# Kernel optimization log

Hardware: AMD Instinct MI355X
Metric: run time of the kernel (lower is better)

The kernel has to match this reference:

```python
import jax, jax.numpy as jnp
import numpy as np

D_MODEL = 1024
D_STATE = 16
EXPAND = 2
D_INNER = D_MODEL * EXPAND
BATCH = 512
SEQ = 100
DT = 0.01


def setup_inputs() -> dict:
    key = jax.random.key(0)
    ks = jax.random.split(key, 12)
    s = 0.02
    log_ts = jnp.linspace(jnp.log(0.001), jnp.log(0.1), D_STATE).reshape(1, D_STATE)
    return {
        "x": jax.random.normal(ks[0], (BATCH, SEQ, D_MODEL), jnp.float32),
        "pos_emb": jax.random.normal(ks[1], (1, 100, D_MODEL), jnp.float32),
        "W_in": jax.random.normal(ks[2], (D_INNER, D_MODEL), jnp.float32) * s,
        "b_in": jnp.zeros((D_INNER,), jnp.float32),
        "W_gate": jax.random.normal(ks[3], (D_INNER, D_MODEL), jnp.float32) * s,
        "b_gate": jnp.zeros((D_INNER,), jnp.float32),
        "A_log": log_ts.astype(jnp.float32),
        "W_B": jax.random.normal(ks[4], (D_STATE, D_INNER), jnp.float32) * s,
        "b_B": jnp.zeros((D_STATE,), jnp.float32),
        "W_C": jax.random.normal(ks[5], (D_STATE, D_MODEL), jnp.float32) * s,
        "b_C": jnp.zeros((D_STATE,), jnp.float32),
        "W_out": jax.random.normal(ks[6], (D_MODEL, D_INNER), jnp.float32) * s,
        "b_out": jnp.zeros((D_MODEL,), jnp.float32),
    }


def reference(x, pos_emb, W_in, b_in, W_gate, b_gate, A_log, W_B, b_B, W_C, b_C, W_out, b_out):
    b, s, _ = x.shape
    d_inner = W_in.shape[0]
    d_state = A_log.shape[-1]
    x = x + pos_emb[:, :s, :]
    x_proj = jnp.einsum("bsd,id->bsi", x, W_in) + b_in
    gate = jax.nn.sigmoid(jnp.einsum("bsd,id->bsi", x, W_gate) + b_gate)
    x_gated = x_proj * gate
    B = jnp.einsum("bsi,ni->bsn", x_gated, W_B) + b_B   # (b, s, d_state)
    C = jnp.einsum("bsd,nd->bsn", x, W_C) + b_C         # (b, s, d_state)
    A = jnp.exp(DT * jnp.exp(A_log))                      # (1, d_state), broadcasts over batch

    def step(h, bc):
        Bt, Ct = bc
        h = A * h + Bt
        return h, h * Ct

    h0 = jnp.zeros((b, d_state), x.dtype)
    _, ys = jax.lax.scan(step, h0, (jnp.swapaxes(B, 0, 1), jnp.swapaxes(C, 0, 1)))
    y = jnp.swapaxes(ys, 0, 1)                            # (b, s, d_state)
    d_slice = min(d_state, d_inner)
    expanded = jnp.pad(y[:, :, :d_slice], ((0, 0), (0, 0), (0, d_inner - d_slice)))
    return jnp.einsum("bsi,di->bsd", expanded, W_out) + b_out
```

## Files before the change

### kernel.cpp

```cpp
#include <hip/hip_runtime.h>
#include <hip/hip_bf16.h>
#include <stdint.h>

typedef unsigned short u16;
typedef u16   u16x8 __attribute__((ext_vector_type(8)));
typedef short s16x8 __attribute__((ext_vector_type(8)));
typedef float f32x4 __attribute__((ext_vector_type(4)));

#define TOKENS 51200
#define DMODEL 1024
#define DINNER 2048
#define NSTATE 16
#define SEQLEN 100

#define OFF_XP    0ull
#define OFF_WCAT  104857600ull
#define OFF_WB    113246208ull
#define OFF_WC    113311744ull
#define OFF_BPART 113344512ull
#define OFF_BFIN  165773312ull
#define OFF_CBUF  169050112ull
#define OFF_Y     172326912ull

__device__ __forceinline__ u16 f2b(float f) {
  uint32_t u = __float_as_uint(f);
  uint32_t r = (u + 0x7fffu + ((u >> 16) & 1u)) >> 16;
  return (u16)r;
}
__device__ __forceinline__ float b2f(u16 u) {
  return __uint_as_float(((uint32_t)u) << 16);
}

#define GLL(gp, lp) __builtin_amdgcn_global_load_lds( \
    (__attribute__((address_space(1))) unsigned int*)(gp), \
    (__attribute__((address_space(3))) unsigned int*)(lp), 16, 0, 0)
#define SB0() __builtin_amdgcn_sched_barrier(0)

__global__ void k_prep_x(const float* __restrict__ x, const float* __restrict__ pos,
                         u16* __restrict__ xp) {
  long e = ((long)blockIdx.x * blockDim.x + threadIdx.x) * 8;
  int d = (int)(e & (DMODEL - 1));
  long tok = e >> 10;
  int s = (int)(tok % SEQLEN);
  f32x4 a0 = *(const f32x4*)(x + e);
  f32x4 a1 = *(const f32x4*)(x + e + 4);
  f32x4 p0 = *(const f32x4*)(pos + (size_t)s * DMODEL + d);
  f32x4 p1 = *(const f32x4*)(pos + (size_t)s * DMODEL + d + 4);
  u16x8 o;
  o[0] = f2b(a0[0] + p0[0]); o[1] = f2b(a0[1] + p0[1]);
  o[2] = f2b(a0[2] + p0[2]); o[3] = f2b(a0[3] + p0[3]);
  o[4] = f2b(a1[0] + p1[0]); o[5] = f2b(a1[1] + p1[1]);
  o[6] = f2b(a1[2] + p1[2]); o[7] = f2b(a1[3] + p1[3]);
  *(u16x8*)(xp + e) = o;
}

__global__ void k_prep_w(const float* __restrict__ Win, const float* __restrict__ Wg,
                         u16* __restrict__ w2) {
  long e = ((long)blockIdx.x * blockDim.x + threadIdx.x) * 8;
  int r = (int)(e >> 10), c = (int)(e & 1023);
  int srow = ((r >> 5) << 4) + (r & 15);
  const float* src = ((r & 16) ? Wg : Win) + (size_t)srow * DMODEL + c;
  f32x4 a0 = *(const f32x4*)src;
  f32x4 a1 = *(const f32x4*)(src + 4);
  u16x8 o;
  o[0] = f2b(a0[0]); o[1] = f2b(a0[1]); o[2] = f2b(a0[2]); o[3] = f2b(a0[3]);
  o[4] = f2b(a1[0]); o[5] = f2b(a1[1]); o[6] = f2b(a1[2]); o[7] = f2b(a1[3]);
  *(u16x8*)(w2 + e) = o;
}

__global__ void k_prep_wbc(const float* __restrict__ WB, const float* __restrict__ WC,
                           u16* __restrict__ wb, u16* __restrict__ wc) {
  long e = ((long)blockIdx.x * blockDim.x + threadIdx.x) * 8;
  const float* src; u16* dst;
  if (e < 32768) { src = WB + e; dst = wb + e; }
  else           { src = WC + (e - 32768); dst = wc + (e - 32768); }
  f32x4 a0 = *(const f32x4*)src;
  f32x4 a1 = *(const f32x4*)(src + 4);
  u16x8 o;
  o[0] = f2b(a0[0]); o[1] = f2b(a0[1]); o[2] = f2b(a0[2]); o[3] = f2b(a0[3]);
  o[4] = f2b(a1[0]); o[5] = f2b(a1[1]); o[6] = f2b(a1[2]); o[7] = f2b(a1[3]);
  *(u16x8*)(dst) = o;
}

__global__ __launch_bounds__(512, 4) void k_gemm256(
    const u16* __restrict__ XP, const u16* __restrict__ W2, const u16* __restrict__ WBb,
    const float* __restrict__ b_in, const float* __restrict__ b_gate,
    float* __restrict__ Bpart) {
  extern __shared__ __align__(16) u16 smem[];
  char* smemc = (char*)smem;

  const int tid = threadIdx.x;
  const int bid = blockIdx.x;
  const int xcd = bid & 7;
  const int q   = bid >> 3;
  const int rb  = xcd * 50 + (q >> 4);
  const int nb  = q & 15;
  const int m0 = rb << 7;
  const int n0 = nb << 8;

  const int srow = tid >> 2;
  const int csrc = ((tid & 3) ^ ((tid >> 3) & 3)) << 3;
  const u16* gA = XP + (size_t)(m0 + srow) * DMODEL + csrc;
  const u16* gB = W2 + (size_t)(n0 + srow) * DMODEL + csrc;
  const int ldst = tid << 3;

  const int wid = tid >> 6, lane = tid & 63;
  const int wm = wid >> 2, wn = wid & 3;
  const int l15 = lane & 15, lhi = lane >> 4;
  const int arow0 = (wm << 6) + l15;
  const int brow0 = (wn << 6) + l15;
  const int kchA = (lhi ^ ((arow0 >> 1) & 3)) << 4;
  const int kchB = (lhi ^ ((brow0 >> 1) & 3)) << 4;

  auto rdA = [&](int bufb, int m) -> s16x8 {
    return *(const s16x8*)(smemc + bufb + ((arow0 + (m << 4)) << 6) + kchA);
  };
  auto rdB = [&](int bufb, int n) -> s16x8 {
    return *(const s16x8*)(smemc + bufb + 8192 + ((brow0 + (n << 4)) << 6) + kchB);
  };
  auto stage = [&](int t) {
    const int bb = (t & 1) << 14;
    const u16* a_ = gA + ((size_t)t << 5);
    const u16* b_ = gB + ((size_t)t << 5);
    GLL(a_,          smem + bb + ldst);
    GLL(b_,          smem + bb + 4096 + ldst);
    GLL(b_ + 131072, smem + bb + 8192 + ldst);
  };

  f32x4 acc[4][4] = {};

  stage(0); stage(1);

#pragma unroll 1
  for (int t = 0; t < 32; ++t) {
    if (t == 31) asm volatile("s_waitcnt vmcnt(0)" ::: "memory");
    else         asm volatile("s_waitcnt vmcnt(3)" ::: "memory");
    SB0();
    asm volatile("s_barrier" ::: "memory");
    SB0();
    const int bufb = (t & 1) << 15;

    s16x8 a[4], b[4];
#pragma unroll
    for (int m = 0; m < 4; ++m) a[m] = rdA(bufb, m);
#pragma unroll
    for (int n = 0; n < 4; ++n) b[n] = rdB(bufb, n);

    __builtin_amdgcn_s_setprio(1);
#pragma unroll
    for (int m = 0; m < 4; ++m)
#pragma unroll
      for (int n = 0; n < 2; ++n)
        acc[m][n] = __builtin_amdgcn_mfma_f32_16x16x32_bf16(a[m], b[n], acc[m][n], 0, 0, 0);
    __builtin_amdgcn_s_setprio(0);

    asm volatile("s_waitcnt lgkmcnt(0)" ::: "memory");
    SB0();
    asm volatile("s_barrier" ::: "memory");
    SB0();
    if (t < 30) stage(t + 2);
    SB0();

    __builtin_amdgcn_s_setprio(1);
#pragma unroll
    for (int m = 0; m < 4; ++m)
#pragma unroll
      for (int n = 2; n < 4; ++n)
        acc[m][n] = __builtin_amdgcn_mfma_f32_16x16x32_bf16(a[m], b[n], acc[m][n], 0, 0, 0);
    __builtin_amdgcn_s_setprio(0);
  }

  asm volatile("s_waitcnt lgkmcnt(0)" ::: "memory");
  SB0();
  asm volatile("s_barrier" ::: "memory");
  SB0();

  u16* xg = smem;
  float bi[2], bg[2];
#pragma unroll
  for (int u = 0; u < 2; ++u) {
    const int gcol = (nb << 7) + (((wn << 1) + u) << 4) + l15;
    bi[u] = b_in[gcol];
    bg[u] = b_gate[gcol];
  }
#pragma unroll
  for (int m = 0; m < 4; ++m)
#pragma unroll
    for (int u = 0; u < 2; ++u)
#pragma unroll
      for (int j = 0; j < 4; ++j) {
        const int row = (wm << 6) + (m << 4) + (lhi << 2) + j;
        const int col = (((wn << 1) + u) << 4) + l15;
        float pv = acc[m][2 * u][j] + bi[u];
        float gv = acc[m][2 * u + 1][j] + bg[u];
        xg[row * 136 + col] = f2b(pv / (1.0f + __expf(-gv)));
      }
  asm volatile("s_waitcnt lgkmcnt(0)" ::: "memory");
  asm volatile("s_barrier" ::: "memory");

  f32x4 bacc = {};
#pragma unroll
  for (int kc = 0; kc < 4; ++kc) {
    s16x8 av = *(const s16x8*)(xg + ((wid << 4) + l15) * 136 + (kc << 5) + (lhi << 3));
    s16x8 bv = *(const s16x8*)(WBb + (size_t)l15 * DINNER + (nb << 7) + (kc << 5) + (lhi << 3));
    bacc = __builtin_amdgcn_mfma_f32_16x16x32_bf16(av, bv, bacc, 0, 0, 0);
  }
  float* outp = Bpart + ((size_t)nb * TOKENS + m0 + (wid << 4) + (lhi << 2)) * NSTATE + l15;
#pragma unroll
  for (int j = 0; j < 4; ++j) outp[j * NSTATE] = bacc[j];
}

__global__ __launch_bounds__(256) void k_C(const u16* __restrict__ XP, const u16* __restrict__ WC,
                                           const float* __restrict__ bC, float* __restrict__ Cb) {
  __shared__ __align__(16) u16 wcl[16 * 1032];
  const int tid = threadIdx.x;
  const int m0 = blockIdx.x << 6;
#pragma unroll
  for (int i = 0; i < 8; ++i) {
    int c = i * 256 + tid;
    int row = c >> 7, col = c & 127;
    *(u16x8*)(wcl + row * 1032 + (col << 3)) = *(const u16x8*)(WC + (row << 10) + (col << 3));
  }
  __syncthreads();
  const int wv = tid >> 6, lane = tid & 63;
  const int l15 = lane & 15, lhi = lane >> 4;
  const u16* xr = XP + (size_t)(m0 + (wv << 4) + l15) * DMODEL + (lhi << 3);
  const u16* wr = wcl + l15 * 1032 + (lhi << 3);
  f32x4 acc = {};
#pragma unroll
  for (int t = 0; t < 32; ++t) {
    s16x8 av = *(const s16x8*)(xr + t * 32);
    s16x8 bv = *(const s16x8*)(wr + t * 32);
    acc = __builtin_amdgcn_mfma_f32_16x16x32_bf16(av, bv, acc, 0, 0, 0);
  }
  const float bc = bC[l15];
  float* o = Cb + (size_t)(m0 + (wv << 4) + (lhi << 2)) * NSTATE + l15;
#pragma unroll
  for (int j = 0; j < 4; ++j) o[j * NSTATE] = acc[j] + bc;
}

__global__ void k_finB(const float* __restrict__ Bpart, const float* __restrict__ bB,
                       float* __restrict__ Bf) {
  const long i = (long)blockIdx.x * blockDim.x + threadIdx.x;
  f32x4 s = {};
#pragma unroll
  for (int cb = 0; cb < 16; ++cb)
    s += *(const f32x4*)(Bpart + (size_t)cb * (TOKENS * NSTATE) + i * 4);
  s += *(const f32x4*)(bB + ((i & 3) << 2));
  *(f32x4*)(Bf + i * 4) = s;
}

__global__ void k_scan(const float* __restrict__ Bf, const float* __restrict__ Cb,
                       const float* __restrict__ Alog, float* __restrict__ Y) {
  const int t = threadIdx.x;
  const int b = blockIdx.x * 16 + (t >> 4);
  const int n = t & 15;
  const float A = __expf(0.01f * __expf(Alog[n]));
  float h = 0.f;
  const size_t base = (size_t)b * SEQLEN * NSTATE + n;
  for (int s = 0; s < SEQLEN; ++s) {
    const size_t idx = base + (size_t)s * NSTATE;
    h = A * h + Bf[idx];
    Y[idx] = h * Cb[idx];
  }
}

__global__ __launch_bounds__(256) void k_out(const float* __restrict__ Y,
                                             const float* __restrict__ Wout,
                                             const float* __restrict__ bout,
                                             float* __restrict__ out) {
  __shared__ float ys[32][16];
  const int tid = threadIdx.x;
  const long t0 = (long)blockIdx.x * 32;
  for (int i = tid; i < 512; i += 256) ys[i >> 4][i & 15] = Y[t0 * 16 + i];
  const int d0 = tid << 2;
  float w[4][16];
#pragma unroll
  for (int j = 0; j < 4; ++j)
#pragma unroll
    for (int q = 0; q < 4; ++q) {
      f32x4 wv = *(const f32x4*)(Wout + (size_t)(d0 + j) * DINNER + q * 4);
#pragma unroll
      for (int e = 0; e < 4; ++e) w[j][q * 4 + e] = wv[e];
    }
  f32x4 bo = *(const f32x4*)(bout + d0);
  __syncthreads();
  for (int r = 0; r < 32; ++r) {
    f32x4 acc = bo;
#pragma unroll
    for (int n = 0; n < 16; ++n) {
      const float yv = ys[r][n];
      acc[0] += yv * w[0][n];
      acc[1] += yv * w[1][n];
      acc[2] += yv * w[2][n];
      acc[3] += yv * w[3][n];
    }
    *(f32x4*)(out + (t0 + r) * 1024 + d0) = acc;
  }
}

extern "C" void kernel_launch(void* const* d_in, const int* in_sizes, int n_in,
                              void* d_out, int out_size, void* d_ws, size_t ws_size,
                              hipStream_t stream) {
  const float* x    = (const float*)d_in[0];
  const float* pos  = (const float*)d_in[1];
  const float* Win  = (const float*)d_in[2];
  const float* bin  = (const float*)d_in[3];
  const float* Wg   = (const float*)d_in[4];
  const float* bg   = (const float*)d_in[5];
  const float* Alog = (const float*)d_in[6];
  const float* WB   = (const float*)d_in[7];
  const float* bB   = (const float*)d_in[8];
  const float* WC   = (const float*)d_in[9];
  const float* bC   = (const float*)d_in[10];
  const float* Wout = (const float*)d_in[11];
  const float* bout = (const float*)d_in[12];

  char* ws = (char*)d_ws;
  u16*   XP   = (u16*)(ws + OFF_XP);
  u16*   W2   = (u16*)(ws + OFF_WCAT);
  u16*   WBb  = (u16*)(ws + OFF_WB);
  u16*   WCb  = (u16*)(ws + OFF_WC);
  float* BP   = (float*)(ws + OFF_BPART);
  float* BF   = (float*)(ws + OFF_BFIN);
  float* CB   = (float*)(ws + OFF_CBUF);
  float* Yb   = (float*)(ws + OFF_Y);

  hipFuncSetAttribute((const void*)k_gemm256,
                      hipFuncAttributeMaxDynamicSharedMemorySize, 65536);

  k_prep_x  <<<25600, 256, 0, stream>>>(x, pos, XP);
  k_prep_w  <<<2048, 256, 0, stream>>>(Win, Wg, W2);
  k_prep_wbc<<<24, 256, 0, stream>>>(WB, WC, WBb, WCb);
  k_gemm256 <<<6400, 512, 65536, stream>>>(XP, W2, WBb, bin, bg, BP);
  k_C       <<<800, 256, 0, stream>>>(XP, WCb, bC, CB);
  k_finB    <<<800, 256, 0, stream>>>(BP, bB, BF);
  k_scan    <<<32, 256, 0, stream>>>(BF, CB, Alog, Yb);
  k_out     <<<1600, 256, 0, stream>>>(Yb, Wout, bout, (float*)d_out);
}
```

Before: 607.0 us.

## Enlarge GEMM tile to 256x256 with 1024 threads and 4-stage LDS pipeline

```diff
diff --git a/kernel.cpp b/kernel.cpp
--- a/kernel.cpp
+++ b/kernel.cpp
@@ -82,7 +82,7 @@
   *(u16x8*)(dst) = o;
 }
 
-__global__ __launch_bounds__(512, 4) void k_gemm256(
+__global__ __launch_bounds__(1024, 4) void k_gemm256(
     const u16* __restrict__ XP, const u16* __restrict__ W2, const u16* __restrict__ WBb,
     const float* __restrict__ b_in, const float* __restrict__ b_gate,
     float* __restrict__ Bpart) {
@@ -91,11 +91,9 @@
 
   const int tid = threadIdx.x;
   const int bid = blockIdx.x;
-  const int xcd = bid & 7;
-  const int q   = bid >> 3;
-  const int rb  = xcd * 50 + (q >> 4);
-  const int nb  = q & 15;
-  const int m0 = rb << 7;
+  const int nb = ((bid & 7) << 1) | ((bid >> 3) & 1);
+  const int rb = bid >> 4;
+  const int m0 = rb << 8;
   const int n0 = nb << 8;
 
   const int srow = tid >> 2;
@@ -107,65 +105,50 @@
   const int wid = tid >> 6, lane = tid & 63;
   const int wm = wid >> 2, wn = wid & 3;
   const int l15 = lane & 15, lhi = lane >> 4;
-  const int arow0 = (wm << 6) + l15;
-  const int brow0 = (wn << 6) + l15;
-  const int kchA = (lhi ^ ((arow0 >> 1) & 3)) << 4;
-  const int kchB = (lhi ^ ((brow0 >> 1) & 3)) << 4;
-
-  auto rdA = [&](int bufb, int m) -> s16x8 {
-    return *(const s16x8*)(smemc + bufb + ((arow0 + (m << 4)) << 6) + kchA);
+  const int kch = (lhi ^ ((l15 >> 1) & 3)) << 4;
+
+  auto rdA = [&](int slotb, int m) -> s16x8 {
+    return *(const s16x8*)(smemc + slotb + (((wm << 6) + (m << 4) + l15) << 6) + kch);
   };
-  auto rdB = [&](int bufb, int n) -> s16x8 {
-    return *(const s16x8*)(smemc + bufb + 8192 + ((brow0 + (n << 4)) << 6) + kchB);
+  auto rdB = [&](int slotb, int n) -> s16x8 {
+    return *(const s16x8*)(smemc + slotb + 16384 + (((wn << 6) + (n << 4) + l15) << 6) + kch);
   };
-  auto stage = [&](int t) {
-    const int bb = (t & 1) << 14;
+  auto STG = [&](int t) {
+    u16* d = smem + ((t & 3) << 14) + ldst;
     const u16* a_ = gA + ((size_t)t << 5);
     const u16* b_ = gB + ((size_t)t << 5);
-    GLL(a_,          smem + bb + ldst);
-    GLL(b_,          smem + bb + 4096 + ldst);
-    GLL(b_ + 131072, smem + bb + 8192 + ldst);
+    GLL(a_, d);
+    GLL(b_, d + 8192);
   };
 
   f32x4 acc[4][4] = {};
 
-  stage(0); stage(1);
+  STG(0); STG(1); STG(2);
 
 #pragma unroll 1
   for (int t = 0; t < 32; ++t) {
-    if (t == 31) asm volatile("s_waitcnt vmcnt(0)" ::: "memory");
-    else         asm volatile("s_waitcnt vmcnt(3)" ::: "memory");
+    asm volatile("s_waitcnt lgkmcnt(0)" ::: "memory");
+    if (t < 30)       asm volatile("s_waitcnt vmcnt(4)" ::: "memory");
+    else if (t == 30) asm volatile("s_waitcnt vmcnt(2)" ::: "memory");
+    else              asm volatile("s_waitcnt vmcnt(0)" ::: "memory");
     SB0();
     asm volatile("s_barrier" ::: "memory");
     SB0();
-    const int bufb = (t & 1) << 15;
+    const int slotb = (t & 3) << 15;
 
     s16x8 a[4], b[4];
 #pragma unroll
-    for (int m = 0; m < 4; ++m) a[m] = rdA(bufb, m);
-#pragma unroll
-    for (int n = 0; n < 4; ++n) b[n] = rdB(bufb, n);
+    for (int m = 0; m < 4; ++m) a[m] = rdA(slotb, m);
+#pragma unroll
+    for (int n = 0; n < 4; ++n) b[n] = rdB(slotb, n);
+    if (t < 29) STG(t + 3);
+    SB0();
 
     __builtin_amdgcn_s_setprio(1);
 #pragma unroll
     for (int m = 0; m < 4; ++m)
 #pragma unroll
-      for (int n = 0; n < 2; ++n)
-        acc[m][n] = __builtin_amdgcn_mfma_f32_16x16x32_bf16(a[m], b[n], acc[m][n], 0, 0, 0);
-    __builtin_amdgcn_s_setprio(0);
-
-    asm volatile("s_waitcnt lgkmcnt(0)" ::: "memory");
-    SB0();
-    asm volatile("s_barrier" ::: "memory");
-    SB0();
-    if (t < 30) stage(t + 2);
-    SB0();
-
-    __builtin_amdgcn_s_setprio(1);
-#pragma unroll
-    for (int m = 0; m < 4; ++m)
-#pragma unroll
-      for (int n = 2; n < 4; ++n)
+      for (int n = 0; n < 4; ++n)
         acc[m][n] = __builtin_amdgcn_mfma_f32_16x16x32_bf16(a[m], b[n], acc[m][n], 0, 0, 0);
     __builtin_amdgcn_s_setprio(0);
   }
@@ -179,7 +162,7 @@
   float bi[2], bg[2];
 #pragma unroll
   for (int u = 0; u < 2; ++u) {
-    const int gcol = (nb << 7) + (((wn << 1) + u) << 4) + l15;
+    const int gcol = (nb << 7) + (wn << 5) + (u << 4) + l15;
     bi[u] = b_in[gcol];
     bg[u] = b_gate[gcol];
   }
@@ -190,7 +173,7 @@
 #pragma unroll
       for (int j = 0; j < 4; ++j) {
         const int row = (wm << 6) + (m << 4) + (lhi << 2) + j;
-        const int col = (((wn << 1) + u) << 4) + l15;
+        const int col = (wn << 5) + (u << 4) + l15;
         float pv = acc[m][2 * u][j] + bi[u];
         float gv = acc[m][2 * u + 1][j] + bg[u];
         xg[row * 136 + col] = f2b(pv / (1.0f + __expf(-gv)));
@@ -327,12 +310,12 @@
   float* Yb   = (float*)(ws + OFF_Y);
 
   hipFuncSetAttribute((const void*)k_gemm256,
-                      hipFuncAttributeMaxDynamicSharedMemorySize, 65536);
+                      hipFuncAttributeMaxDynamicSharedMemorySize, 131072);
 
   k_prep_x  <<<25600, 256, 0, stream>>>(x, pos, XP);
   k_prep_w  <<<2048, 256, 0, stream>>>(Win, Wg, W2);
   k_prep_wbc<<<24, 256, 0, stream>>>(WB, WC, WBb, WCb);
-  k_gemm256 <<<6400, 512, 65536, stream>>>(XP, W2, WBb, bin, bg, BP);
+  k_gemm256 <<<3200, 1024, 131072, stream>>>(XP, W2, WBb, bin, bg, BP);
   k_C       <<<800, 256, 0, stream>>>(XP, WCb, bC, CB);
   k_finB    <<<800, 256, 0, stream>>>(BP, bB, BF);
   k_scan    <<<32, 256, 0, stream>>>(BF, CB, Alog, Yb);
```

After: 601.4 us. No clear change (-0.9%).
